# Kernel tuning notes

Measured on AMD Instinct MI355X. Metric: run time of the kernel, lower is better.

The kernel has to match this reference:

```python
import jax, jax.numpy as jnp
import numpy as np

B, N, D, K, M = 4, 12500, 128, 8, 20  # batch, nodes, dim, num_caps, neighbors per node
EPS = 1e-12  # torch F.normalize eps


def _l2norm(v, axis):
    return v / jnp.maximum(jnp.linalg.norm(v, axis=axis, keepdims=True), EPS)


def setup_inputs() -> dict:
    key = jax.random.key(0)
    k1, k2 = jax.random.split(key)
    n = B * N
    input_ = jax.random.normal(k1, (B, N, D), dtype=jnp.float32)
    # original code gathers z[neighbors + arange//20*5] from an (n+1)-row table
    # (row n is the zero pad). Generate valid final indices and pre-subtract the
    # offset so the in-reference index math lands in [0, n].
    offset = (jnp.arange(n * M, dtype=jnp.int32) // 20) * 5
    target = jax.random.randint(k2, (n * M,), 0, n + 1, dtype=jnp.int32)
    neighbors = target - offset
    return {"input_": input_, "neighbors": neighbors, "max_iter": 3}


def reference(input_, neighbors, max_iter):
    b, nn_, d = input_.shape
    n = b * nn_
    k = K
    dd = d // k
    m = neighbors.shape[0] // n

    # per-capsule L2 normalize
    x = _l2norm(input_.reshape(n, k, dd), axis=2)  # [n, k, dd]

    # gather neighbor capsules (with zero-pad row at index n)
    z_tab = jnp.concatenate([x.reshape(n, d), jnp.zeros((1, d), x.dtype)], axis=0)
    idx = neighbors + (jnp.arange(neighbors.shape[0], dtype=neighbors.dtype) // 20) * 5
    z = z_tab[idx].reshape(n, m, k, dd)  # [n, m, k, dd]

    u = None
    for it in range(max_iter):
        if u is None:
            p = jnp.zeros((n, m, k), x.dtype)
        else:
            p = jnp.einsum('nmkd,nkd->nmk', z, u)
        p = jax.nn.softmax(p, axis=2)
        u = jnp.einsum('nmkd,nmk->nkd', z, p) + x
        if it < max_iter - 1:
            u = _l2norm(u, axis=2)
    return u.reshape(b, nn_, d)
```

## Files before the change

kernel.cpp:

```cpp
#include <hip/hip_runtime.h>


#define D   128
#define K   8
#define DD  16
#define M   20

typedef _Float16 h2 __attribute__((ext_vector_type(2)));
typedef unsigned int u32;

__device__ __forceinline__ h2 pack_h2(float a, float b) {
    return __builtin_bit_cast(h2, __builtin_amdgcn_cvt_pkrtz(a, b));
}

#define DPPADD(x, ctrl) ((x) + __int_as_float(__builtin_amdgcn_update_dpp( \
        0, __float_as_int(x), (ctrl), 0xF, 0xF, false)))

__device__ __forceinline__ float red8_b(float x) {
    x = DPPADD(x, 0xB1); x = DPPADD(x, 0x4E); x = DPPADD(x, 0x141);
    return x;
}

#define RED8_X4(a, b, c, d) \
  asm volatile( \
    "s_nop 1\n\t" \
    "v_add_f32_dpp %0, %0, %0 quad_perm:[1,0,3,2] row_mask:0xf bank_mask:0xf\n\t" \
    "v_add_f32_dpp %1, %1, %1 quad_perm:[1,0,3,2] row_mask:0xf bank_mask:0xf\n\t" \
    "v_add_f32_dpp %2, %2, %2 quad_perm:[1,0,3,2] row_mask:0xf bank_mask:0xf\n\t" \
    "v_add_f32_dpp %3, %3, %3 quad_perm:[1,0,3,2] row_mask:0xf bank_mask:0xf\n\t" \
    "v_add_f32_dpp %0, %0, %0 quad_perm:[2,3,0,1] row_mask:0xf bank_mask:0xf\n\t" \
    "v_add_f32_dpp %1, %1, %1 quad_perm:[2,3,0,1] row_mask:0xf bank_mask:0xf\n\t" \
    "v_add_f32_dpp %2, %2, %2 quad_perm:[2,3,0,1] row_mask:0xf bank_mask:0xf\n\t" \
    "v_add_f32_dpp %3, %3, %3 quad_perm:[2,3,0,1] row_mask:0xf bank_mask:0xf\n\t" \
    "v_add_f32_dpp %0, %0, %0 row_half_mirror row_mask:0xf bank_mask:0xf\n\t" \
    "v_add_f32_dpp %1, %1, %1 row_half_mirror row_mask:0xf bank_mask:0xf\n\t" \
    "v_add_f32_dpp %2, %2, %2 row_half_mirror row_mask:0xf bank_mask:0xf\n\t" \
    "v_add_f32_dpp %3, %3, %3 row_half_mirror row_mask:0xf bank_mask:0xf" \
    : "+v"(a), "+v"(b), "+v"(c), "+v"(d))

__device__ __forceinline__ float dot2(u32 za, h2 ub) {
#if __has_builtin(__builtin_amdgcn_fdot2)
    return __builtin_amdgcn_fdot2(__builtin_bit_cast(h2, za), ub, 0.0f, false);
#else
    h2 ah = __builtin_bit_cast(h2, za);
    return fmaf((float)ah.x, (float)ub.x, (float)ah.y * (float)ub.y);
#endif
}

__global__ __launch_bounds__(256) void prenorm2_kernel(const float* __restrict__ in,
                                                       u32* __restrict__ tab,
                                                       int totalPairs) {
    int i = blockIdx.x * 256 + threadIdx.x;
    float2 v = make_float2(0.0f, 0.0f);
    if (i < totalPairs) v = ((const float2*)in)[i];
    float ss = red8_b(v.x * v.x + v.y * v.y);
    float inv = (ss > 0.0f) ? rsqrtf(ss) : 0.0f;
    if (i < totalPairs + D / 2)
        tab[i] = __builtin_bit_cast(u32, pack_h2(v.x * inv, v.y * inv));
}

template<bool PRE>
__global__ __launch_bounds__(256) void routing_kernel(
    const _Float16* __restrict__ tab,
    const float*    __restrict__ raw,
    const int*      __restrict__ nbr,
    const int*      __restrict__ maxit_p,
    float*          __restrict__ out,
    int n)
{
    const int t  = threadIdx.x;
    const int wv = t >> 6;
    const int l  = t & 63;
    const int node = blockIdx.x * 4 + wv;
    const int myk  = l >> 3;
    if (node >= n) return;
    const int max_iter = maxit_p[0];
    const int nodeu = __builtin_amdgcn_readfirstlane(node);

    __shared__ float p_lds[4][M][K];
    __shared__ u32   w_lds[4][M][K];

    int ids[M];
    {
        const int* nrow = nbr + nodeu * M;
        #pragma unroll
        for (int mm = 0; mm < M; ++mm) ids[mm] = nrow[mm] + nodeu * 5;
    }

    u32 z[M];
    h2  xh;
    if (PRE) {
        const u32* t32 = (const u32*)tab;
        xh = __builtin_bit_cast(h2, t32[(size_t)nodeu * (D / 2) + l]);
        #pragma unroll
        for (int mm = 0; mm < M; ++mm)
            z[mm] = t32[(size_t)ids[mm] * (D / 2) + l];
    } else {
        const float2* r2 = (const float2*)raw;
        float2 x0 = r2[(size_t)nodeu * (D / 2) + l];
        float s = red8_b(x0.x * x0.x + x0.y * x0.y);
        float inv = (s > 0.0f) ? rsqrtf(s) : 0.0f;
        xh = pack_h2(x0.x * inv, x0.y * inv);
        #pragma unroll
        for (int mm = 0; mm < M; ++mm) {
            float2 zv = (ids[mm] < n) ? r2[(size_t)ids[mm] * (D / 2) + l]
                                      : make_float2(0.f, 0.f);
            float s2 = red8_b(zv.x * zv.x + zv.y * zv.y);
            float i2 = (s2 > 0.0f) ? rsqrtf(s2) : 0.0f;
            z[mm] = __builtin_bit_cast(u32, pack_h2(zv.x * i2, zv.y * i2));
        }
    }

    const h2 kEighth = pack_h2(0.125f, 0.125f);
    h2 u = xh;
    #pragma unroll
    for (int mm = 0; mm < M; ++mm)
        u = __builtin_bit_cast(h2, z[mm]) * kEighth + u;
    if (max_iter > 1) {
        float s = red8_b(dot2(__builtin_bit_cast(u32, u), u));
        float inv = (s > 0.0f) ? rsqrtf(s) : 0.0f;
        h2 invh = pack_h2(inv, inv);
        u = u * invh;
    }

    for (int it = 1; it < max_iter; ++it) {
        #pragma unroll
        for (int mm = 0; mm < M; mm += 4) {
            float p0 = dot2(z[mm + 0], u);
            float p1 = dot2(z[mm + 1], u);
            float p2 = dot2(z[mm + 2], u);
            float p3 = dot2(z[mm + 3], u);
            RED8_X4(p0, p1, p2, p3);
            if ((l & 7) == 0) {
                p_lds[wv][mm + 0][myk] = p0;
                p_lds[wv][mm + 1][myk] = p1;
                p_lds[wv][mm + 2][myk] = p2;
                p_lds[wv][mm + 3][myk] = p3;
            }
        }
        __builtin_amdgcn_wave_barrier();

        #pragma unroll
        for (int base = 0; base < M; base += 8) {
            int mm = base + (l >> 3);
            int mc = (mm < M) ? mm : (M - 1);
            float e = __expf(p_lds[wv][mc][l & 7]);
            float S = red8_b(e);
            float w = e * __builtin_amdgcn_rcpf(S);
            if (mm < M)
                w_lds[wv][mm][l & 7] = __builtin_bit_cast(u32, pack_h2(w, w));
        }
        __builtin_amdgcn_wave_barrier();

        h2 unew = xh;
        #pragma unroll
        for (int mm = 0; mm < M; ++mm) {
            h2 w2 = __builtin_bit_cast(h2, w_lds[wv][mm][myk]);
            unew = __builtin_bit_cast(h2, z[mm]) * w2 + unew;
        }
        u = unew;
        if (it < max_iter - 1) {
            float s = red8_b(dot2(__builtin_bit_cast(u32, u), u));
            float inv = (s > 0.0f) ? rsqrtf(s) : 0.0f;
            h2 invh = pack_h2(inv, inv);
            u = u * invh;
        }
        __builtin_amdgcn_wave_barrier();
    }

    float2* o2 = (float2*)out;
    o2[(size_t)node * (D / 2) + l] = make_float2((float)u.x, (float)u.y);
}

extern "C" void kernel_launch(void* const* d_in, const int* in_sizes, int n_in,
                              void* d_out, int out_size, void* d_ws, size_t ws_size,
                              hipStream_t stream) {
    const float* in  = (const float*)d_in[0];
    const int*   nbr = (const int*)d_in[1];
    const int*   mit = (const int*)d_in[2];
    float*       out = (float*)d_out;

    const int n     = in_sizes[0] / D;
    const int total = n * D;
    const int nblk  = (n + 3) / 4;

    if (ws_size >= (size_t)(total + D) * sizeof(_Float16)) {
        _Float16* tab = (_Float16*)d_ws;
        const int totalPairs = total / 2;
        const int tblk = (totalPairs + D / 2 + 255) / 256;
        prenorm2_kernel<<<tblk, 256, 0, stream>>>(in, (u32*)tab, totalPairs);
        routing_kernel<true><<<nblk, 256, 0, stream>>>(tab, nullptr, nbr, mit, out, n);
    } else {
        routing_kernel<false><<<nblk, 256, 0, stream>>>(nullptr, in, nbr, mit, out, n);
    }
}
```

Measured before the change: 49.79 us.

## Use a persistent grid-stride routing kernel with double-buffered neighbor gathers

```diff
diff --git a/kernel.cpp b/kernel.cpp
--- a/kernel.cpp
+++ b/kernel.cpp
@@ -59,57 +59,26 @@
         tab[i] = __builtin_bit_cast(u32, pack_h2(v.x * inv, v.y * inv));
 }
 
-template<bool PRE>
-__global__ __launch_bounds__(256) void routing_kernel(
-    const _Float16* __restrict__ tab,
-    const float*    __restrict__ raw,
-    const int*      __restrict__ nbr,
-    const int*      __restrict__ maxit_p,
-    float*          __restrict__ out,
-    int n)
+__device__ __forceinline__ void load_node(const u32* __restrict__ t32,
+                                          const int* __restrict__ nbr,
+                                          int node, int l,
+                                          u32* z, u32& xw) {
+    const int nodeu = __builtin_amdgcn_readfirstlane(node);
+    const int* nrow = nbr + nodeu * M;
+    xw = t32[(size_t)nodeu * (D / 2) + l];
+    #pragma unroll
+    for (int mm = 0; mm < M; ++mm) {
+        int idx = nrow[mm] + nodeu * 5;
+        z[mm] = t32[(size_t)idx * (D / 2) + l];
+    }
+}
+
+__device__ __forceinline__ void compute_node(
+    const u32* z, u32 xw, int max_iter, int wv, int l, int myk,
+    float (*p_lds)[M][K], u32 (*w_lds)[M][K],
+    float* __restrict__ out, int node)
 {
-    const int t  = threadIdx.x;
-    const int wv = t >> 6;
-    const int l  = t & 63;
-    const int node = blockIdx.x * 4 + wv;
-    const int myk  = l >> 3;
-    if (node >= n) return;
-    const int max_iter = maxit_p[0];
-    const int nodeu = __builtin_amdgcn_readfirstlane(node);
-
-    __shared__ float p_lds[4][M][K];
-    __shared__ u32   w_lds[4][M][K];
-
-    int ids[M];
-    {
-        const int* nrow = nbr + nodeu * M;
-        #pragma unroll
-        for (int mm = 0; mm < M; ++mm) ids[mm] = nrow[mm] + nodeu * 5;
-    }
-
-    u32 z[M];
-    h2  xh;
-    if (PRE) {
-        const u32* t32 = (const u32*)tab;
-        xh = __builtin_bit_cast(h2, t32[(size_t)nodeu * (D / 2) + l]);
-        #pragma unroll
-        for (int mm = 0; mm < M; ++mm)
-            z[mm] = t32[(size_t)ids[mm] * (D / 2) + l];
-    } else {
-        const float2* r2 = (const float2*)raw;
-        float2 x0 = r2[(size_t)nodeu * (D / 2) + l];
-        float s = red8_b(x0.x * x0.x + x0.y * x0.y);
-        float inv = (s > 0.0f) ? rsqrtf(s) : 0.0f;
-        xh = pack_h2(x0.x * inv, x0.y * inv);
-        #pragma unroll
-        for (int mm = 0; mm < M; ++mm) {
-            float2 zv = (ids[mm] < n) ? r2[(size_t)ids[mm] * (D / 2) + l]
-                                      : make_float2(0.f, 0.f);
-            float s2 = red8_b(zv.x * zv.x + zv.y * zv.y);
-            float i2 = (s2 > 0.0f) ? rsqrtf(s2) : 0.0f;
-            z[mm] = __builtin_bit_cast(u32, pack_h2(zv.x * i2, zv.y * i2));
-        }
-    }
+    const h2 xh = __builtin_bit_cast(h2, xw);
 
     const h2 kEighth = pack_h2(0.125f, 0.125f);
     h2 u = xh;
@@ -119,8 +88,7 @@
     if (max_iter > 1) {
         float s = red8_b(dot2(__builtin_bit_cast(u32, u), u));
         float inv = (s > 0.0f) ? rsqrtf(s) : 0.0f;
-        h2 invh = pack_h2(inv, inv);
-        u = u * invh;
+        u = u * pack_h2(inv, inv);
     }
 
     for (int it = 1; it < max_iter; ++it) {
@@ -162,14 +130,94 @@
         if (it < max_iter - 1) {
             float s = red8_b(dot2(__builtin_bit_cast(u32, u), u));
             float inv = (s > 0.0f) ? rsqrtf(s) : 0.0f;
-            h2 invh = pack_h2(inv, inv);
-            u = u * invh;
+            u = u * pack_h2(inv, inv);
         }
         __builtin_amdgcn_wave_barrier();
     }
 
     float2* o2 = (float2*)out;
     o2[(size_t)node * (D / 2) + l] = make_float2((float)u.x, (float)u.y);
+}
+
+__global__ __launch_bounds__(256) void routing_pipe_kernel(
+    const _Float16* __restrict__ tab,
+    const int*      __restrict__ nbr,
+    const int*      __restrict__ maxit_p,
+    float*          __restrict__ out,
+    int n, int W)
+{
+    const int t  = threadIdx.x;
+    const int wv = t >> 6;
+    const int l  = t & 63;
+    const int myk = l >> 3;
+    const int max_iter = maxit_p[0];
+    const u32* t32 = (const u32*)tab;
+
+    __shared__ float p_lds[4][M][K];
+    __shared__ u32   w_lds[4][M][K];
+
+    u32 zA[M], zB[M], xwA, xwB;
+
+    int iA = blockIdx.x * 4 + wv;
+    if (iA >= n) return;
+    load_node(t32, nbr, iA, l, zA, xwA);
+    int iB = iA + W;
+
+    for (;;) {
+        if (iB < n) load_node(t32, nbr, iB, l, zB, xwB);
+        compute_node(zA, xwA, max_iter, wv, l, myk, p_lds, w_lds, out, iA);
+        iA = iB + W;
+        if (iB >= n) break;
+        if (iA < n) load_node(t32, nbr, iA, l, zA, xwA);
+        compute_node(zB, xwB, max_iter, wv, l, myk, p_lds, w_lds, out, iB);
+        iB = iA + W;
+        if (iA >= n) break;
+    }
+}
+
+__global__ __launch_bounds__(256) void routing_raw_kernel(
+    const float* __restrict__ raw,
+    const int*   __restrict__ nbr,
+    const int*   __restrict__ maxit_p,
+    float*       __restrict__ out,
+    int n)
+{
+    const int t  = threadIdx.x;
+    const int wv = t >> 6;
+    const int l  = t & 63;
+    const int node = blockIdx.x * 4 + wv;
+    const int myk  = l >> 3;
+    if (node >= n) return;
+    const int max_iter = maxit_p[0];
+    const int nodeu = __builtin_amdgcn_readfirstlane(node);
+
+    __shared__ float p_lds[4][M][K];
+    __shared__ u32   w_lds[4][M][K];
+
+    int ids[M];
+    {
+        const int* nrow = nbr + nodeu * M;
+        #pragma unroll
+        for (int mm = 0; mm < M; ++mm) ids[mm] = nrow[mm] + nodeu * 5;
+    }
+
+    u32 z[M], xw;
+    {
+        const float2* r2 = (const float2*)raw;
+        float2 x0 = r2[(size_t)nodeu * (D / 2) + l];
+        float s = red8_b(x0.x * x0.x + x0.y * x0.y);
+        float inv = (s > 0.0f) ? rsqrtf(s) : 0.0f;
+        xw = __builtin_bit_cast(u32, pack_h2(x0.x * inv, x0.y * inv));
+        #pragma unroll
+        for (int mm = 0; mm < M; ++mm) {
+            float2 zv = (ids[mm] < n) ? r2[(size_t)ids[mm] * (D / 2) + l]
+                                      : make_float2(0.f, 0.f);
+            float s2 = red8_b(zv.x * zv.x + zv.y * zv.y);
+            float i2 = (s2 > 0.0f) ? rsqrtf(s2) : 0.0f;
+            z[mm] = __builtin_bit_cast(u32, pack_h2(zv.x * i2, zv.y * i2));
+        }
+    }
+    compute_node(z, xw, max_iter, wv, l, myk, p_lds, w_lds, out, node);
 }
 
 extern "C" void kernel_launch(void* const* d_in, const int* in_sizes, int n_in,
@@ -182,15 +230,16 @@
 
     const int n     = in_sizes[0] / D;
     const int total = n * D;
-    const int nblk  = (n + 3) / 4;
 
     if (ws_size >= (size_t)(total + D) * sizeof(_Float16)) {
         _Float16* tab = (_Float16*)d_ws;
         const int totalPairs = total / 2;
         const int tblk = (totalPairs + D / 2 + 255) / 256;
         prenorm2_kernel<<<tblk, 256, 0, stream>>>(in, (u32*)tab, totalPairs);
-        routing_kernel<true><<<nblk, 256, 0, stream>>>(tab, nullptr, nbr, mit, out, n);
+        const int nblk = 1024;
+        const int W    = nblk * 4;
+        routing_pipe_kernel<<<nblk, 256, 0, stream>>>(tab, nbr, mit, out, n, W);
     } else {
-        routing_kernel<false><<<nblk, 256, 0, stream>>>(nullptr, in, nbr, mit, out, n);
-    }
-}
+        routing_raw_kernel<<<(n + 3) / 4, 256, 0, stream>>>(in, nbr, mit, out, n);
+    }
+}
```

Measured after the change: 64.68 us. +29.9%, slower.
